# Performance work log

Measured on AMD Instinct MI355X. Metric: run time of the kernel, lower is better.

## Reference

```python
import jax, jax.numpy as jnp
import numpy as np


def setup_inputs() -> dict:
    B, n, C = 256, 512, 256
    key = jax.random.key(0)
    ks = jax.random.split(key, 8)
    s = 1.0 / np.sqrt(C)
    return {
        "P": jax.random.normal(ks[0], (B, n, C), dtype=jnp.float32),
        "id": jax.random.randint(ks[1], (B,), 0, n, dtype=jnp.int64),
        "Wq": jax.random.normal(ks[2], (C, C), dtype=jnp.float32) * s,
        "bq": jax.random.normal(ks[3], (C,), dtype=jnp.float32) * s,
        "Wk": jax.random.normal(ks[4], (C, C), dtype=jnp.float32) * s,
        "bk": jax.random.normal(ks[5], (C,), dtype=jnp.float32) * s,
        "Wv": jax.random.normal(ks[6], (C, C), dtype=jnp.float32) * s,
        "bv": jax.random.normal(ks[7], (C,), dtype=jnp.float32) * s,
    }


def reference(P, id, Wq, bq, Wk, bk, Wv, bv):
    # Gather the query row per batch first, then project (same math as
    # projecting all rows and gathering, but avoids redundant compute).
    B = P.shape[0]
    p_sel = P[jnp.arange(B), id]                 # [B, C]
    Q = p_sel @ Wq.T + bq                        # [B, C]
    K = jnp.einsum('bnc,dc->bnd', P, Wk) + bk    # [B, n, C]
    V = jnp.einsum('bnc,dc->bnd', P, Wv) + bv    # [B, n, C]
    scores = jnp.einsum('bc,bnc->bn', Q, K)      # [B, n] (no sqrt scaling, per source)
    attn = jax.nn.softmax(scores, axis=-1)       # [B, n]
    out = jnp.einsum('bn,bnc->bc', attn, V)      # [B, C]
    return out
```

## Files before the change

kernel.cpp:

```cpp
#include <hip/hip_runtime.h>

#define BATCH 256
#define NROW  512
#define CDIM  256
#define WAVES 8
#define RPW   (NROW / WAVES)
#define CHK   8
#define NCHK  (RPW / CHK)

__global__ __launch_bounds__(512) void attn_one_kernel(
    const float* __restrict__ P, const int* __restrict__ idx,
    const float* __restrict__ Wq, const float* __restrict__ bq,
    const float* __restrict__ Wk, const float* __restrict__ Wv,
    const float* __restrict__ bv, float* __restrict__ out) {
  const int b = blockIdx.x;
  const int t = threadIdx.x;
  const int lane = t & 63;
  const int w = t >> 6;

  __shared__ float s_psel[CDIM];
  __shared__ float s_q[CDIM];
  __shared__ float s_qk[CDIM];
  __shared__ float s_ctx[WAVES][CDIM];
  __shared__ float s_m[WAVES], s_l[WAVES];
  __shared__ float s_ctxn[CDIM];
  __shared__ float s_part[2][CDIM];

  const float* Pw = P + ((size_t)b * NROW + (size_t)w * RPW) * CDIM;

  float4 pv0[CHK], pv1[CHK];
#pragma unroll
  for (int i = 0; i < CHK; ++i)
    pv0[i] = ((const float4*)(Pw + (size_t)i * CDIM))[lane];

  if (t < CDIM)
    s_psel[t] = P[((size_t)b * NROW + (size_t)idx[b]) * CDIM + t];
  __syncthreads();

  if (t < CDIM) {
    const float4* wq4 = (const float4*)(Wq + (size_t)t * CDIM);
    const float4* ps4 = (const float4*)s_psel;
    float acc = 0.f;
#pragma unroll 8
    for (int c4 = 0; c4 < CDIM / 4; ++c4) {
      float4 wv = wq4[c4], p = ps4[c4];
      acc += wv.x * p.x + wv.y * p.y + wv.z * p.z + wv.w * p.w;
    }
    s_q[t] = acc + bq[t];
  }
  __syncthreads();

  if (t < CDIM) {
    float acc = 0.f;
#pragma unroll 8
    for (int d = 0; d < CDIM; ++d) acc += s_q[d] * Wk[(size_t)d * CDIM + t];
    s_qk[t] = acc;
  }
  __syncthreads();

  const float4 qk4 = ((const float4*)s_qk)[lane];

  float m = -1e30f, l = 0.f;
  float4 ctx = make_float4(0.f, 0.f, 0.f, 0.f);

#define PREFETCH(dst, chn)                                                   \
  {                                                                          \
    _Pragma("unroll") for (int i = 0; i < CHK; ++i) dst[i] =                 \
        ((const float4*)(Pw + (size_t)((chn)*CHK + i) * CDIM))[lane];        \
  }

#define CONSUME(cur)                                                         \
  {                                                                          \
    float sc[CHK];                                                           \
    _Pragma("unroll") for (int i = 0; i < CHK; ++i) {                        \
      float part = cur[i].x * qk4.x + cur[i].y * qk4.y +                     \
                   cur[i].z * qk4.z + cur[i].w * qk4.w;                      \
      _Pragma("unroll") for (int mm = 32; mm >= 1; mm >>= 1)                 \
          part += __shfl_xor(part, mm, 64);                                  \
      sc[i] = part;                                                          \
    }                                                                        \
    float cmax = sc[0];                                                      \
    _Pragma("unroll") for (int i = 1; i < CHK; ++i)                          \
        cmax = fmaxf(cmax, sc[i]);                                           \
    const float mnew = fmaxf(m, cmax);                                       \
    const float scale = __expf(m - mnew);       \
    l *= scale;                                                              \
    ctx.x *= scale; ctx.y *= scale; ctx.z *= scale; ctx.w *= scale;          \
    _Pragma("unroll") for (int i = 0; i < CHK; ++i) {                        \
      const float p = __expf(sc[i] - mnew);                                  \
      l += p;                                                                \
      ctx.x += p * cur[i].x; ctx.y += p * cur[i].y;                          \
      ctx.z += p * cur[i].z; ctx.w += p * cur[i].w;                          \
    }                                                                        \
    m = mnew;                                                                \
  }

#pragma unroll
  for (int cc = 0; cc < NCHK; cc += 2) {
    if (cc + 1 < NCHK) PREFETCH(pv1, cc + 1);
    CONSUME(pv0);
    if (cc + 2 < NCHK) PREFETCH(pv0, cc + 2);
    if (cc + 1 < NCHK) CONSUME(pv1);
  }
#undef PREFETCH
#undef CONSUME

  ((float4*)s_ctx[w])[lane] = ctx;
  if (lane == 0) { s_m[w] = m; s_l[w] = l; }
  __syncthreads();

  if (t < CDIM) {
    float mg = s_m[0];
#pragma unroll
    for (int i = 1; i < WAVES; ++i) mg = fmaxf(mg, s_m[i]);
    float lg = 0.f, c = 0.f;
#pragma unroll
    for (int i = 0; i < WAVES; ++i) {
      const float co = __expf(s_m[i] - mg);
      lg += co * s_l[i];
      c  += co * s_ctx[i][t];
    }
    s_ctxn[t] = c / lg;
  }
  __syncthreads();

  {
    const int d = t & (CDIM - 1);
    const int h = t >> 8;
    const float4* wv4 =
        (const float4*)(Wv + (size_t)d * CDIM + (size_t)h * (CDIM / 2));
    const float4* cx4 = (const float4*)(s_ctxn + h * (CDIM / 2));
    float acc = 0.f;
#pragma unroll 8
    for (int j = 0; j < CDIM / 8; ++j) {
      float4 wv = wv4[j], cc = cx4[j];
      acc += wv.x * cc.x + wv.y * cc.y + wv.z * cc.z + wv.w * cc.w;
    }
    s_part[h][d] = acc;
  }
  __syncthreads();
  if (t < CDIM)
    out[(size_t)b * CDIM + t] = s_part[0][t] + s_part[1][t] + bv[t];
}

extern "C" void kernel_launch(void* const* d_in, const int* in_sizes, int n_in,
                              void* d_out, int out_size, void* d_ws,
                              size_t ws_size, hipStream_t stream) {
  const float* P  = (const float*)d_in[0];
  const int*  idx = (const int*)d_in[1];
  const float* Wq = (const float*)d_in[2];
  const float* bq = (const float*)d_in[3];
  const float* Wk = (const float*)d_in[4];
  const float* Wv = (const float*)d_in[6];
  const float* bv = (const float*)d_in[7];
  float* out = (float*)d_out;

  attn_one_kernel<<<BATCH, 512, 0, stream>>>(P, idx, Wq, bq, Wk, Wv, bv, out);
}
```

Baseline: 234.3 us.

## Split attention into qk, split-K partial softmax, and combine kernels

Replaces the single per-batch kernel with three kernels. The first computes q and qk per batch with wave-level coalesced reductions. The second splits each batch's 512 rows across 8 blocks, so 2048 blocks run the online softmax and stream P. The third merges the partials and applies Wv. This raises parallelism and memory-level concurrency for streaming the 128MB P tensor, at the cost of two extra launches and workspace traffic for the partials.

```diff
diff --git a/kernel.cpp b/kernel.cpp
--- a/kernel.cpp
+++ b/kernel.cpp
@@ -3,16 +3,19 @@
 #define BATCH 256
 #define NROW  512
 #define CDIM  256
-#define WAVES 8
-#define RPW   (NROW / WAVES)
-#define CHK   8
+#define SPLIT 8
+#define CHUNK (NROW / SPLIT)
+#define WPB   4
+#define RPW   (CHUNK / WPB)
+#define CHK   4
 #define NCHK  (RPW / CHK)
 
-__global__ __launch_bounds__(512) void attn_one_kernel(
+#define DOT4(a, b) ((a).x * (b).x + (a).y * (b).y + (a).z * (b).z + (a).w * (b).w)
+
+__global__ __launch_bounds__(256) void qk_kernel(
     const float* __restrict__ P, const int* __restrict__ idx,
     const float* __restrict__ Wq, const float* __restrict__ bq,
-    const float* __restrict__ Wk, const float* __restrict__ Wv,
-    const float* __restrict__ bv, float* __restrict__ out) {
+    const float* __restrict__ Wk, float* __restrict__ qk) {
   const int b = blockIdx.x;
   const int t = threadIdx.x;
   const int lane = t & 63;
@@ -20,45 +23,70 @@
 
   __shared__ float s_psel[CDIM];
   __shared__ float s_q[CDIM];
-  __shared__ float s_qk[CDIM];
-  __shared__ float s_ctx[WAVES][CDIM];
-  __shared__ float s_m[WAVES], s_l[WAVES];
-  __shared__ float s_ctxn[CDIM];
-  __shared__ float s_part[2][CDIM];
-
-  const float* Pw = P + ((size_t)b * NROW + (size_t)w * RPW) * CDIM;
+  __shared__ float s_qkp[WPB][CDIM];
+
+  s_psel[t] = P[((size_t)b * NROW + (size_t)idx[b]) * CDIM + t];
+  __syncthreads();
+
+  const float4 pr4 = ((const float4*)s_psel)[lane];
+
+  const int d0 = w * 64;
+#pragma unroll
+  for (int g = 0; g < 8; ++g) {
+    float4 wq[8];
+#pragma unroll
+    for (int i = 0; i < 8; ++i)
+      wq[i] = ((const float4*)(Wq + (size_t)(d0 + g * 8 + i) * CDIM))[lane];
+#pragma unroll
+    for (int i = 0; i < 8; ++i) {
+      float part = DOT4(wq[i], pr4);
+#pragma unroll
+      for (int mm = 32; mm >= 1; mm >>= 1) part += __shfl_xor(part, mm, 64);
+      if (lane == 0) s_q[d0 + g * 8 + i] = part + bq[d0 + g * 8 + i];
+    }
+  }
+  __syncthreads();
+
+  {
+    float4 acc = make_float4(0.f, 0.f, 0.f, 0.f);
+#pragma unroll 8
+    for (int dd = 0; dd < 64; ++dd) {
+      const int d = d0 + dd;
+      const float qd = s_q[d];
+      const float4 wk4 = ((const float4*)(Wk + (size_t)d * CDIM))[lane];
+      acc.x += qd * wk4.x; acc.y += qd * wk4.y;
+      acc.z += qd * wk4.z; acc.w += qd * wk4.w;
+    }
+    ((float4*)s_qkp[w])[lane] = acc;
+  }
+  __syncthreads();
+
+  qk[(size_t)b * CDIM + t] =
+      s_qkp[0][t] + s_qkp[1][t] + s_qkp[2][t] + s_qkp[3][t];
+}
+
+__global__ __launch_bounds__(256, 8) void attn_part_kernel(
+    const float* __restrict__ P, const float* __restrict__ qk,
+    float* __restrict__ ctxp, float* __restrict__ mp, float* __restrict__ lp) {
+  const int bs = blockIdx.x;
+  const int b = bs >> 3;
+  const int s = bs & (SPLIT - 1);
+  const int t = threadIdx.x;
+  const int lane = t & 63;
+  const int w = t >> 6;
+
+  __shared__ float s_ctx[WPB][CDIM];
+  __shared__ float s_m[WPB], s_l[WPB];
+
+  const float* Pw =
+      P + ((size_t)b * NROW + (size_t)s * CHUNK + (size_t)w * RPW) * CDIM;
 
   float4 pv0[CHK], pv1[CHK];
 #pragma unroll
   for (int i = 0; i < CHK; ++i)
     pv0[i] = ((const float4*)(Pw + (size_t)i * CDIM))[lane];
 
-  if (t < CDIM)
-    s_psel[t] = P[((size_t)b * NROW + (size_t)idx[b]) * CDIM + t];
-  __syncthreads();
-
-  if (t < CDIM) {
-    const float4* wq4 = (const float4*)(Wq + (size_t)t * CDIM);
-    const float4* ps4 = (const float4*)s_psel;
-    float acc = 0.f;
-#pragma unroll 8
-    for (int c4 = 0; c4 < CDIM / 4; ++c4) {
-      float4 wv = wq4[c4], p = ps4[c4];
-      acc += wv.x * p.x + wv.y * p.y + wv.z * p.z + wv.w * p.w;
-    }
-    s_q[t] = acc + bq[t];
-  }
-  __syncthreads();
-
-  if (t < CDIM) {
-    float acc = 0.f;
-#pragma unroll 8
-    for (int d = 0; d < CDIM; ++d) acc += s_q[d] * Wk[(size_t)d * CDIM + t];
-    s_qk[t] = acc;
-  }
-  __syncthreads();
-
-  const float4 qk4 = ((const float4*)s_qk)[lane];
+  const float4 qk4 = ((const float4*)(qk + (size_t)b * CDIM))[lane];
 
   float m = -1e30f, l = 0.f;
   float4 ctx = make_float4(0.f, 0.f, 0.f, 0.f);
@@ -66,15 +94,14 @@
 #define PREFETCH(dst, chn)                                                   \
   {                                                                          \
     _Pragma("unroll") for (int i = 0; i < CHK; ++i) dst[i] =                 \
-        ((const float4*)(Pw + (size_t)((chn)*CHK + i) * CDIM))[lane];        \
+        ((const float4*)(Pw + (size_t)((chn) * CHK + i) * CDIM))[lane];      \
   }
 
 #define CONSUME(cur)                                                         \
   {                                                                          \
     float sc[CHK];                                                           \
     _Pragma("unroll") for (int i = 0; i < CHK; ++i) {                        \
-      float part = cur[i].x * qk4.x + cur[i].y * qk4.y +                     \
-                   cur[i].z * qk4.z + cur[i].w * qk4.w;                      \
+      float part = DOT4(cur[i], qk4);                                        \
       _Pragma("unroll") for (int mm = 32; mm >= 1; mm >>= 1)                 \
           part += __shfl_xor(part, mm, 64);                                  \
       sc[i] = part;                                                          \
@@ -109,38 +136,70 @@
   if (lane == 0) { s_m[w] = m; s_l[w] = l; }
   __syncthreads();
 
-  if (t < CDIM) {
-    float mg = s_m[0];
-#pragma unroll
-    for (int i = 1; i < WAVES; ++i) mg = fmaxf(mg, s_m[i]);
-    float lg = 0.f, c = 0.f;
-#pragma unroll
-    for (int i = 0; i < WAVES; ++i) {
-      const float co = __expf(s_m[i] - mg);
-      lg += co * s_l[i];
-      c  += co * s_ctx[i][t];
-    }
+  float mb = fmaxf(fmaxf(s_m[0], s_m[1]), fmaxf(s_m[2], s_m[3]));
+  float co0 = __expf(s_m[0] - mb), co1 = __expf(s_m[1] - mb);
+  float co2 = __expf(s_m[2] - mb), co3 = __expf(s_m[3] - mb);
+  ctxp[(size_t)bs * CDIM + t] = co0 * s_ctx[0][t] + co1 * s_ctx[1][t] +
+                                co2 * s_ctx[2][t] + co3 * s_ctx[3][t];
+  if (t == 0) {
+    mp[bs] = mb;
+    lp[bs] = co0 * s_l[0] + co1 * s_l[1] + co2 * s_l[2] + co3 * s_l[3];
+  }
+}
+
+__global__ __launch_bounds__(256) void combine_kernel(
+    const float* __restrict__ ctxp, const float* __restrict__ mp,
+    const float* __restrict__ lp, const float* __restrict__ Wv,
+    const float* __restrict__ bv, float* __restrict__ out) {
+  const int b = blockIdx.x;
+  const int t = threadIdx.x;
+  const int lane = t & 63;
+  const int w = t >> 6;
+
+  __shared__ float s_ctxn[CDIM];
+
+  {
+    float ms[SPLIT];
+    float mg = -3.4e38f;
+#pragma unroll
+    for (int i = 0; i < SPLIT; ++i) {
+      ms[i] = mp[b * SPLIT + i];
+      mg = fmaxf(mg, ms[i]);
+    }
+    float ww[SPLIT];
+    float lg = 0.f;
+#pragma unroll
+    for (int i = 0; i < SPLIT; ++i) {
+      ww[i] = __expf(ms[i] - mg);
+      lg += lp[b * SPLIT + i] * ww[i];
+    }
+    float c = 0.f;
+#pragma unroll
+    for (int i = 0; i < SPLIT; ++i)
+      c += ctxp[(size_t)(b * SPLIT + i) * CDIM + t] * ww[i];
     s_ctxn[t] = c / lg;
   }
   __syncthreads();
 
-  {
-    const int d = t & (CDIM - 1);
-    const int h = t >> 8;
-    const float4* wv4 =
-        (const float4*)(Wv + (size_t)d * CDIM + (size_t)h * (CDIM / 2));
-    const float4* cx4 = (const float4*)(s_ctxn + h * (CDIM / 2));
-    float acc = 0.f;
-#pragma unroll 8
-    for (int j = 0; j < CDIM / 8; ++j) {
-      float4 wv = wv4[j], cc = cx4[j];
-      acc += wv.x * cc.x + wv.y * cc.y + wv.z * cc.z + wv.w * cc.w;
-    }
-    s_part[h][d] = acc;
-  }
-  __syncthreads();
-  if (t < CDIM)
-    out[(size_t)b * CDIM + t] = s_part[0][t] + s_part[1][t] + bv[t];
+  const float4 cx4 = ((const float4*)s_ctxn)[lane];
+  const int d0 = w * 64;
+#pragma unroll
+  for (int g = 0; g < 8; ++g) {
+    float4 wv[8];
+#pragma unroll
+    for (int i = 0; i < 8; ++i)
+      wv[i] = ((const float4*)(Wv + (size_t)(d0 + g * 8 + i) * CDIM))[lane];
+#pragma unroll
+    for (int i = 0; i < 8; ++i) {
+      float part = DOT4(wv[i], cx4);
+#pragma unroll
+      for (int mm = 32; mm >= 1; mm >>= 1) part += __shfl_xor(part, mm, 64);
+      if (lane == 0) {
+        const int d = d0 + g * 8 + i;
+        out[(size_t)b * CDIM + d] = part + bv[d];
+      }
+    }
+  }
 }
 
 extern "C" void kernel_launch(void* const* d_in, const int* in_sizes, int n_in,
@@ -155,5 +214,13 @@
   const float* bv = (const float*)d_in[7];
   float* out = (float*)d_out;
 
-  attn_one_kernel<<<BATCH, 512, 0, stream>>>(P, idx, Wq, bq, Wk, Wv, bv, out);
-}
+  float* ws   = (float*)d_ws;
+  float* qk   = ws;
+  float* ctxp = qk + BATCH * CDIM;
+  float* mp   = ctxp + BATCH * SPLIT * CDIM;
+  float* lp   = mp + BATCH * SPLIT;
+
+  qk_kernel<<<BATCH, 256, 0, stream>>>(P, idx, Wq, bq, Wk, qk);
+  attn_part_kernel<<<BATCH * SPLIT, 256, 0, stream>>>(P, qk, ctxp, mp, lp);
+  combine_kernel<<<BATCH, 256, 0, stream>>>(ctxp, mp, lp, Wv, bv, out);
+}
```

Result: slower. 256.1 us (+9.3%).

## Use 16 waves per block and wave-cooperative coalesced projections

Applied to the files above, without the earlier changes.

Doubles the block to 1024 threads (16 waves), so each wave streams 32 rows of P instead of 64. The Q, qK and V projections are rewritten so that all waves share the work. Each wave reads whole weight rows coalesced as float4 and reduces them with shuffles, replacing the old per-thread strided dot products that used only half the threads. The cost is more reduction and shuffle overhead and higher register pressure under launch_bounds(1024, 4), which could cause spills with the prefetch buffers.

```diff
diff --git a/kernel.cpp b/kernel.cpp
--- a/kernel.cpp
+++ b/kernel.cpp
@@ -3,12 +3,14 @@
 #define BATCH 256
 #define NROW  512
 #define CDIM  256
-#define WAVES 8
+#define WAVES 16
 #define RPW   (NROW / WAVES)
 #define CHK   8
 #define NCHK  (RPW / CHK)
 
-__global__ __launch_bounds__(512) void attn_one_kernel(
+#define DOT4(a, b) ((a).x * (b).x + (a).y * (b).y + (a).z * (b).z + (a).w * (b).w)
+
+__global__ __launch_bounds__(1024, 4) void attn_mono_kernel(
     const float* __restrict__ P, const int* __restrict__ idx,
     const float* __restrict__ Wq, const float* __restrict__ bq,
     const float* __restrict__ Wk, const float* __restrict__ Wv,
@@ -21,10 +23,9 @@
   __shared__ float s_psel[CDIM];
   __shared__ float s_q[CDIM];
   __shared__ float s_qk[CDIM];
-  __shared__ float s_ctx[WAVES][CDIM];
+  __shared__ float s_wavebuf[WAVES][CDIM];
   __shared__ float s_m[WAVES], s_l[WAVES];
   __shared__ float s_ctxn[CDIM];
-  __shared__ float s_part[2][CDIM];
 
   const float* Pw = P + ((size_t)b * NROW + (size_t)w * RPW) * CDIM;
 
@@ -37,24 +38,44 @@
     s_psel[t] = P[((size_t)b * NROW + (size_t)idx[b]) * CDIM + t];
   __syncthreads();
 
-  if (t < CDIM) {
-    const float4* wq4 = (const float4*)(Wq + (size_t)t * CDIM);
-    const float4* ps4 = (const float4*)s_psel;
-    float acc = 0.f;
-#pragma unroll 8
-    for (int c4 = 0; c4 < CDIM / 4; ++c4) {
-      float4 wv = wq4[c4], p = ps4[c4];
-      acc += wv.x * p.x + wv.y * p.y + wv.z * p.z + wv.w * p.w;
+  const float4 pr4 = ((const float4*)s_psel)[lane];
+  const int d0 = w * 16;
+
+#pragma unroll
+  for (int g = 0; g < 2; ++g) {
+    float4 wq[8];
+#pragma unroll
+    for (int i = 0; i < 8; ++i)
+      wq[i] = ((const float4*)(Wq + (size_t)(d0 + g * 8 + i) * CDIM))[lane];
+#pragma unroll
+    for (int i = 0; i < 8; ++i) {
+      float part = DOT4(wq[i], pr4);
+#pragma unroll
+      for (int mm = 32; mm >= 1; mm >>= 1) part += __shfl_xor(part, mm, 64);
+      if (lane == 0) s_q[d0 + g * 8 + i] = part + bq[d0 + g * 8 + i];
     }
-    s_q[t] = acc + bq[t];
+  }
+  __syncthreads();
+
+  {
+    float4 acc = make_float4(0.f, 0.f, 0.f, 0.f);
+#pragma unroll
+    for (int dd = 0; dd < 16; ++dd) {
+      const int d = d0 + dd;
+      const float qd = s_q[d];
+      const float4 wk4 = ((const float4*)(Wk + (size_t)d * CDIM))[lane];
+      acc.x += qd * wk4.x; acc.y += qd * wk4.y;
+      acc.z += qd * wk4.z; acc.w += qd * wk4.w;
+    }
+    ((float4*)s_wavebuf[w])[lane] = acc;
   }
   __syncthreads();
 
   if (t < CDIM) {
-    float acc = 0.f;
-#pragma unroll 8
-    for (int d = 0; d < CDIM; ++d) acc += s_q[d] * Wk[(size_t)d * CDIM + t];
-    s_qk[t] = acc;
+    float a = 0.f;
+#pragma unroll
+    for (int i = 0; i < WAVES; ++i) a += s_wavebuf[i][t];
+    s_qk[t] = a;
   }
   __syncthreads();
 
@@ -66,15 +87,14 @@
 #define PREFETCH(dst, chn)                                                   \
   {                                                                          \
     _Pragma("unroll") for (int i = 0; i < CHK; ++i) dst[i] =                 \
-        ((const float4*)(Pw + (size_t)((chn)*CHK + i) * CDIM))[lane];        \
+        ((const float4*)(Pw + (size_t)((chn) * CHK + i) * CDIM))[lane];      \
   }
 
 #define CONSUME(cur)                                                         \
   {                                                                          \
     float sc[CHK];                                                           \
     _Pragma("unroll") for (int i = 0; i < CHK; ++i) {                        \
-      float part = cur[i].x * qk4.x + cur[i].y * qk4.y +                     \
-                   cur[i].z * qk4.z + cur[i].w * qk4.w;                      \
+      float part = DOT4(cur[i], qk4);                                        \
       _Pragma("unroll") for (int mm = 32; mm >= 1; mm >>= 1)                 \
           part += __shfl_xor(part, mm, 64);                                  \
       sc[i] = part;                                                          \
@@ -83,7 +103,7 @@
     _Pragma("unroll") for (int i = 1; i < CHK; ++i)                          \
         cmax = fmaxf(cmax, sc[i]);                                           \
     const float mnew = fmaxf(m, cmax);                                       \
-    const float scale = __expf(m - mnew);       \
+    const float scale = __expf(m - mnew);      \
     l *= scale;                                                              \
     ctx.x *= scale; ctx.y *= scale; ctx.z *= scale; ctx.w *= scale;          \
     _Pragma("unroll") for (int i = 0; i < CHK; ++i) {                        \
@@ -105,7 +125,7 @@
 #undef PREFETCH
 #undef CONSUME
 
-  ((float4*)s_ctx[w])[lane] = ctx;
+  ((float4*)s_wavebuf[w])[lane] = ctx;
   if (lane == 0) { s_m[w] = m; s_l[w] = l; }
   __syncthreads();
 
@@ -118,29 +138,32 @@
     for (int i = 0; i < WAVES; ++i) {
       const float co = __expf(s_m[i] - mg);
       lg += co * s_l[i];
-      c  += co * s_ctx[i][t];
+      c  += co * s_wavebuf[i][t];
     }
     s_ctxn[t] = c / lg;
   }
   __syncthreads();
 
   {
-    const int d = t & (CDIM - 1);
-    const int h = t >> 8;
-    const float4* wv4 =
-        (const float4*)(Wv + (size_t)d * CDIM + (size_t)h * (CDIM / 2));
-    const float4* cx4 = (const float4*)(s_ctxn + h * (CDIM / 2));
-    float acc = 0.f;
-#pragma unroll 8
-    for (int j = 0; j < CDIM / 8; ++j) {
-      float4 wv = wv4[j], cc = cx4[j];
-      acc += wv.x * cc.x + wv.y * cc.y + wv.z * cc.z + wv.w * cc.w;
+    const float4 cx4 = ((const float4*)s_ctxn)[lane];
+#pragma unroll
+    for (int g = 0; g < 2; ++g) {
+      float4 wv[8];
+#pragma unroll
+      for (int i = 0; i < 8; ++i)
+        wv[i] = ((const float4*)(Wv + (size_t)(d0 + g * 8 + i) * CDIM))[lane];
+#pragma unroll
+      for (int i = 0; i < 8; ++i) {
+        float part = DOT4(wv[i], cx4);
+#pragma unroll
+        for (int mm = 32; mm >= 1; mm >>= 1) part += __shfl_xor(part, mm, 64);
+        if (lane == 0) {
+          const int d = d0 + g * 8 + i;
+          out[(size_t)b * CDIM + d] = part + bv[d];
+        }
+      }
     }
-    s_part[h][d] = acc;
   }
-  __syncthreads();
-  if (t < CDIM)
-    out[(size_t)b * CDIM + t] = s_part[0][t] + s_part[1][t] + bv[t];
 }
 
 extern "C" void kernel_launch(void* const* d_in, const int* in_sizes, int n_in,
@@ -155,5 +178,6 @@
   const float* bv = (const float*)d_in[7];
   float* out = (float*)d_out;
 
-  attn_one_kernel<<<BATCH, 512, 0, stream>>>(P, idx, Wq, bq, Wk, Wv, bv, out);
+  attn_mono_kernel<<<BATCH, 1024, 0, stream>>>(P, idx, Wq, bq, Wk, Wv, bv,
+                                               out);
 }
```

Result: faster. 223.4 us (-4.7%).
